# Kernel optimization log

Hardware: AMD Instinct MI355X
Metric: run time of the kernel (lower is better)

The kernel has to match this reference:

```python
import jax, jax.numpy as jnp
import numpy as np

R = 16      # num_rels
NB = 16     # num_bases
N2 = 8192   # dp2 neighbours (layer-0 sampled nodes)
N1 = 1024   # dp1 neighbours (layer-1 sampled nodes)
NOUT = 256  # output batch nodes
F = 128     # feat_size
E = 64      # embed_size
C = 32      # num_classes


def setup_inputs() -> dict:
    key = jax.random.key(0)
    ks = jax.random.split(key, 8)
    g = lambda k, sh, scale: jax.random.normal(k, sh, dtype=jnp.float32) * scale
    return {
        "X_batch": g(ks[0], (N2, F), 1.0),
        "sel_idx": jnp.arange(N2, dtype=jnp.int64) if jax.config.jax_enable_x64 else jnp.arange(N2, dtype=jnp.int32),
        "A0": g(ks[1], (N1, R * N2), 1.0 / np.sqrt(R * N2)),
        "A1": g(ks[2], (NOUT, R * N1), 1.0 / np.sqrt(R * N1)),
        "comp1": g(ks[3], (R, NB), 1.0 / np.sqrt(NB)),
        "bases1": g(ks[4], (NB, F, E), 1.0 / np.sqrt(F)),
        "comp2": g(ks[5], (R, NB), 1.0 / np.sqrt(NB)),
        "bases2": g(ks[6], (NB, E, C), 1.0 / np.sqrt(E)),
        "bias1": jnp.zeros((E,), jnp.float32),
        "bias2": jnp.zeros((C,), jnp.float32),
    }


def reference(X_batch, sel_idx, A0, A1, comp1, bases1, comp2, bases2, bias1, bias2):
    # gather the rows of X_batch corresponding to dp2 neighbours
    x = X_batch[sel_idx]                                  # [N2, F]
    # layer 1: basis-composed relation weights, relation-stacked matmul
    w1 = jnp.einsum('rb,beh->reh', comp1, bases1)         # [R, F, E]
    xw = jnp.einsum('ne,reh->rnh', x, w1)                 # [R, N2, E]
    h1 = A0 @ xw.reshape(R * N2, E)                       # [N1, E]
    h1 = jax.nn.relu(h1 + bias1)
    # layer 2
    w2 = jnp.einsum('rb,bho->rho', comp2, bases2)         # [R, E, C]
    h2 = jnp.einsum('nh,rhc->rnc', h1, w2)                # [R, N1, C]
    out = A1 @ h2.reshape(R * N1, C) + bias2              # [NOUT, C]
    return out
```

## Files before the change

kernel.cpp:

```cpp
#include <hip/hip_runtime.h>

#define RR_ 16
#define N2_ 8192
#define N1_ 1024
#define NOUT_ 256
#define F_ 128
#define E_ 64
#define C_ 32
#define KBIG_ 131072

typedef __attribute__((ext_vector_type(4))) float f32x4;
typedef __attribute__((ext_vector_type(8))) short short8;
typedef __attribute__((ext_vector_type(4))) short s16x4;

#define MFMA(a,b,c) __builtin_amdgcn_mfma_f32_16x16x32_bf16((a),(b),(c),0,0,0)

__device__ __forceinline__ unsigned short f2bf(float f) {
  unsigned int u = __builtin_bit_cast(unsigned int, f);
  u += 0x7fffu + ((u >> 16) & 1u);
  return (unsigned short)(u >> 16);
}

__device__ __forceinline__ short8 cvt8(f32x4 v0, f32x4 v1) {
  short8 r;
  r[0] = (short)f2bf(v0[0]); r[1] = (short)f2bf(v0[1]);
  r[2] = (short)f2bf(v0[2]); r[3] = (short)f2bf(v0[3]);
  r[4] = (short)f2bf(v1[0]); r[5] = (short)f2bf(v1[1]);
  r[6] = (short)f2bf(v1[2]); r[7] = (short)f2bf(v1[3]);
  return r;
}

__global__ __launch_bounds__(256) void k_prep(
    const float* __restrict__ comp1, const float* __restrict__ bases1,
    const float* __restrict__ comp2, const float* __restrict__ bases2,
    short* __restrict__ w1T, short* __restrict__ w2T)
{
  int bid = blockIdx.x, t = threadIdx.x;
  if (bid < 32) {
    int base = bid * 4096;
    for (int i = 0; i < 16; ++i) {
      int e = base + i * 256 + t;
      int r = e >> 13, rem = e & 8191;
      int h = rem >> 7, f = rem & 127;
      float s = 0.f;
      #pragma unroll
      for (int b = 0; b < 16; ++b) s += comp1[r * 16 + b] * bases1[b * 8192 + f * 64 + h];
      w1T[e] = (short)f2bf(s);
    }
  } else {
    int base = (bid - 32) * 4096;
    for (int i = 0; i < 16; ++i) {
      int e = base + i * 256 + t;
      int r = e >> 11, rem = e & 2047;
      int c = rem >> 6, h = rem & 63;
      float s = 0.f;
      #pragma unroll
      for (int b = 0; b < 16; ++b) s += comp2[r * 16 + b] * bases2[b * 2048 + h * 32 + c];
      w2T[e] = (short)f2bf(s);
    }
  }
}

__global__ __launch_bounds__(256) void k_xw(
    const float* __restrict__ X, const int* __restrict__ sel,
    const short* __restrict__ w1T, short* __restrict__ xwT)
{
  int w = blockIdx.x * 4 + (threadIdx.x >> 6);
  int lane = threadIdx.x & 63, lr = lane & 15, lg = lane >> 4;
  int r = w >> 8;
  int n0 = (w & 255) * 32;

  bool is64 = (sel[1] == 0 && sel[2] == 1);
  int i0 = is64 ? sel[2 * (n0 + lr)] : sel[n0 + lr];
  int i1 = is64 ? sel[2 * (n0 + 16 + lr)] : sel[n0 + 16 + lr];

  const short* aBase = w1T + r * 8192 + lr * 128 + 8 * lg;
  const float* b0p = X + (size_t)i0 * 128 + 8 * lg;
  const float* b1p = X + (size_t)i1 * 128 + 8 * lg;

  f32x4 acc[4][2] = {};
  #pragma unroll
  for (int ks = 0; ks < 4; ++ks) {
    short8 a[4];
    #pragma unroll
    for (int mf = 0; mf < 4; ++mf)
      a[mf] = *(const short8*)(aBase + mf * 2048 + ks * 32);
    short8 b[2];
    b[0] = cvt8(*(const f32x4*)(b0p + ks * 32), *(const f32x4*)(b0p + ks * 32 + 4));
    b[1] = cvt8(*(const f32x4*)(b1p + ks * 32), *(const f32x4*)(b1p + ks * 32 + 4));
    #pragma unroll
    for (int mf = 0; mf < 4; ++mf)
      #pragma unroll
      for (int nf = 0; nf < 2; ++nf)
        acc[mf][nf] = MFMA(a[mf], b[nf], acc[mf][nf]);
  }
  #pragma unroll
  for (int mf = 0; mf < 4; ++mf)
    #pragma unroll
    for (int nf = 0; nf < 2; ++nf)
      #pragma unroll
      for (int rr = 0; rr < 4; ++rr) {
        int h = mf * 16 + 4 * lg + rr;
        int col = r * 8192 + n0 + nf * 16 + lr;
        xwT[(size_t)h * KBIG_ + col] = (short)f2bf(acc[mf][nf][rr]);
      }
}

__global__ __launch_bounds__(256) void k_h1(
    const float* __restrict__ A0, const short* __restrict__ xwT,
    float* __restrict__ h1p)
{
  int w = blockIdx.x * 4 + (threadIdx.x >> 6);
  int lane = threadIdx.x & 63, lr = lane & 15, lg = lane >> 4;
  int mt = w >> 7;
  int ch = w & 127;
  int m0 = mt * 64;
  size_t kc = (size_t)ch * 1024;

  const float* aBase = A0 + (size_t)(m0 + lr) * KBIG_ + kc + 8 * lg;
  const short* bBase = xwT + (size_t)lr * KBIG_ + kc + 8 * lg;

  f32x4 acc[4][4] = {};
  for (int ks = 0; ks < 32; ++ks) {
    short8 a[4];
    #pragma unroll
    for (int mf = 0; mf < 4; ++mf) {
      const float* p = aBase + (size_t)mf * 16 * KBIG_ + ks * 32;
      f32x4 v0 = __builtin_nontemporal_load((const f32x4*)p);
      f32x4 v1 = __builtin_nontemporal_load((const f32x4*)p + 1);
      a[mf] = cvt8(v0, v1);
    }
    short8 b[4];
    #pragma unroll
    for (int nf = 0; nf < 4; ++nf)
      b[nf] = *(const short8*)(bBase + (size_t)nf * 16 * KBIG_ + ks * 32);
    #pragma unroll
    for (int mf = 0; mf < 4; ++mf)
      #pragma unroll
      for (int nf = 0; nf < 4; ++nf)
        acc[mf][nf] = MFMA(a[mf], b[nf], acc[mf][nf]);
  }
  float* base = h1p + (size_t)ch * 65536;
  #pragma unroll
  for (int mf = 0; mf < 4; ++mf)
    #pragma unroll
    for (int nf = 0; nf < 4; ++nf)
      #pragma unroll
      for (int rr = 0; rr < 4; ++rr)
        base[(m0 + mf * 16 + 4 * lg + rr) * 64 + nf * 16 + lr] = acc[mf][nf][rr];
}

__global__ __launch_bounds__(256) void k_red(
    const float* __restrict__ h1p, const float* __restrict__ bias1,
    short* __restrict__ h1b)
{
  int e = (blockIdx.x * 256 + threadIdx.x) * 4;
  f32x4 s = {0.f, 0.f, 0.f, 0.f};
  #pragma unroll 8
  for (int c = 0; c < 128; ++c) {
    f32x4 v = *(const f32x4*)(h1p + (size_t)c * 65536 + e);
    s += v;
  }
  int h = e & 63;
  s16x4 o;
  #pragma unroll
  for (int j = 0; j < 4; ++j) {
    float x = s[j] + bias1[h + j];
    x = x > 0.f ? x : 0.f;
    o[j] = (short)f2bf(x);
  }
  *(s16x4*)(h1b + e) = o;
}

__global__ __launch_bounds__(256) void k_h2(
    const short* __restrict__ w2T, const short* __restrict__ h1b,
    short* __restrict__ H2T)
{
  int w = blockIdx.x * 4 + (threadIdx.x >> 6);
  int lane = threadIdx.x & 63, lr = lane & 15, lg = lane >> 4;
  int r = w >> 4;
  int n0 = (w & 15) * 64;

  f32x4 acc[2][4] = {};
  #pragma unroll
  for (int ks = 0; ks < 2; ++ks) {
    short8 a[2];
    #pragma unroll
    for (int mf = 0; mf < 2; ++mf)
      a[mf] = *(const short8*)(w2T + r * 2048 + (mf * 16 + lr) * 64 + ks * 32 + 8 * lg);
    short8 b[4];
    #pragma unroll
    for (int nf = 0; nf < 4; ++nf)
      b[nf] = *(const short8*)(h1b + (size_t)(n0 + nf * 16 + lr) * 64 + ks * 32 + 8 * lg);
    #pragma unroll
    for (int mf = 0; mf < 2; ++mf)
      #pragma unroll
      for (int nf = 0; nf < 4; ++nf)
        acc[mf][nf] = MFMA(a[mf], b[nf], acc[mf][nf]);
  }
  #pragma unroll
  for (int mf = 0; mf < 2; ++mf)
    #pragma unroll
    for (int nf = 0; nf < 4; ++nf)
      #pragma unroll
      for (int rr = 0; rr < 4; ++rr) {
        int c = mf * 16 + 4 * lg + rr;
        int col = r * 1024 + n0 + nf * 16 + lr;
        H2T[(size_t)c * 16384 + col] = (short)f2bf(acc[mf][nf][rr]);
      }
}

__global__ __launch_bounds__(256) void k_out(
    const float* __restrict__ A1, const short* __restrict__ H2T,
    float* __restrict__ outp)
{
  int w = blockIdx.x * 4 + (threadIdx.x >> 6);
  int lane = threadIdx.x & 63, lr = lane & 15, lg = lane >> 4;
  int mt = w >> 7;
  int ch = w & 127;
  int m0 = mt * 64;
  size_t kc = (size_t)ch * 128;

  const float* aBase = A1 + (size_t)(m0 + lr) * 16384 + kc + 8 * lg;
  const short* bBase = H2T + (size_t)lr * 16384 + kc + 8 * lg;

  f32x4 acc[4][2] = {};
  #pragma unroll
  for (int ks = 0; ks < 4; ++ks) {
    short8 a[4];
    #pragma unroll
    for (int mf = 0; mf < 4; ++mf) {
      const float* p = aBase + (size_t)mf * 16 * 16384 + ks * 32;
      f32x4 v0 = __builtin_nontemporal_load((const f32x4*)p);
      f32x4 v1 = __builtin_nontemporal_load((const f32x4*)p + 1);
      a[mf] = cvt8(v0, v1);
    }
    short8 b[2];
    #pragma unroll
    for (int nf = 0; nf < 2; ++nf)
      b[nf] = *(const short8*)(bBase + (size_t)nf * 16 * 16384 + ks * 32);
    #pragma unroll
    for (int mf = 0; mf < 4; ++mf)
      #pragma unroll
      for (int nf = 0; nf < 2; ++nf)
        acc[mf][nf] = MFMA(a[mf], b[nf], acc[mf][nf]);
  }
  float* base = outp + (size_t)ch * 8192;
  #pragma unroll
  for (int mf = 0; mf < 4; ++mf)
    #pragma unroll
    for (int nf = 0; nf < 2; ++nf)
      #pragma unroll
      for (int rr = 0; rr < 4; ++rr)
        base[(m0 + mf * 16 + 4 * lg + rr) * 32 + nf * 16 + lr] = acc[mf][nf][rr];
}

__global__ __launch_bounds__(256) void k_outred(
    const float* __restrict__ outp, const float* __restrict__ bias2,
    float* __restrict__ out)
{
  int e = (blockIdx.x * 256 + threadIdx.x) * 4;
  f32x4 s = {0.f, 0.f, 0.f, 0.f};
  #pragma unroll 8
  for (int c = 0; c < 128; ++c) {
    f32x4 v = *(const f32x4*)(outp + (size_t)c * 8192 + e);
    s += v;
  }
  int cc = e & 31;
  f32x4 o;
  #pragma unroll
  for (int j = 0; j < 4; ++j)
    o[j] = s[j] + bias2[cc + j];
  *(f32x4*)(out + e) = o;
}

extern "C" void kernel_launch(void* const* d_in, const int* in_sizes, int n_in,
                              void* d_out, int out_size, void* d_ws, size_t ws_size,
                              hipStream_t stream) {
  (void)in_sizes; (void)n_in; (void)out_size; (void)ws_size;
  const float* X      = (const float*)d_in[0];
  const int*   sel    = (const int*)  d_in[1];
  const float* A0     = (const float*)d_in[2];
  const float* A1     = (const float*)d_in[3];
  const float* comp1  = (const float*)d_in[4];
  const float* bases1 = (const float*)d_in[5];
  const float* comp2  = (const float*)d_in[6];
  const float* bases2 = (const float*)d_in[7];
  const float* bias1  = (const float*)d_in[8];
  const float* bias2  = (const float*)d_in[9];
  float* out = (float*)d_out;

  char* ws = (char*)d_ws;
  short* w1T = (short*)(ws);
  short* w2T = (short*)(ws + 262144);
  short* xwT = (short*)(ws + 327680);
  float* h1p = (float*)(ws + 17104896);
  short* h1b = (short*)(ws + 50659328);
  short* H2T = (short*)(ws + 50790400);
  float* outp= (float*)(ws + 51838976);

  k_prep  <<<40,   256, 0, stream>>>(comp1, bases1, comp2, bases2, w1T, w2T);
  k_xw    <<<1024, 256, 0, stream>>>(X, sel, w1T, xwT);
  k_h1    <<<512,  256, 0, stream>>>(A0, xwT, h1p);
  k_red   <<<64,   256, 0, stream>>>(h1p, bias1, h1b);
  k_h2    <<<64,   256, 0, stream>>>(w2T, h1b, H2T);
  k_out   <<<128,  256, 0, stream>>>(A1, H2T, outp);
  k_outred<<<8,    256, 0, stream>>>(outp, bias2, out);
}
```

Before: 254.4 us.

## Stage A0 tiles into LDS with double-buffered async loads in k_h1

Rewrites the big A0 @ xw kernel so each block stages 64x256 fp32 tiles of A0 into double-buffered shared memory using global_load_lds, overlapping the next tile's load with MFMA work on the current one. K is split into 16 chunks instead of 128, which shrinks the partial-sum buffer and the k_red reduction, and the grid is halved. It also switches k_out's A1 loads from nontemporal to regular loads. The trade-off is fewer blocks with 128KB of LDS each (low occupancy), plus a full barrier per stage.

```diff
diff --git a/kernel.cpp b/kernel.cpp
--- a/kernel.cpp
+++ b/kernel.cpp
@@ -106,48 +106,63 @@
       }
 }
 
+__device__ __forceinline__ void stage16(const float* gbase, int s, float* ldst) {
+  #pragma unroll
+  for (int j = 0; j < 16; ++j) {
+    const float* gp = gbase + (size_t)j * KBIG_ + (size_t)s * 256;
+    __builtin_amdgcn_global_load_lds(
+        (const __attribute__((address_space(1))) void*)gp,
+        (__attribute__((address_space(3))) void*)(ldst + j * 256), 16, 0, 0);
+  }
+}
+
 __global__ __launch_bounds__(256) void k_h1(
     const float* __restrict__ A0, const short* __restrict__ xwT,
     float* __restrict__ h1p)
 {
-  int w = blockIdx.x * 4 + (threadIdx.x >> 6);
-  int lane = threadIdx.x & 63, lr = lane & 15, lg = lane >> 4;
-  int mt = w >> 7;
-  int ch = w & 127;
+  __shared__ float As[2][64][256];
+  int tid = threadIdx.x;
+  int w = tid >> 6;
+  int lane = tid & 63, lr = lane & 15, lg = lane >> 4;
+  int mt = blockIdx.x >> 4;
+  int ch = blockIdx.x & 15;
   int m0 = mt * 64;
-  size_t kc = (size_t)ch * 1024;
-
-  const float* aBase = A0 + (size_t)(m0 + lr) * KBIG_ + kc + 8 * lg;
-  const short* bBase = xwT + (size_t)lr * KBIG_ + kc + 8 * lg;
-
-  f32x4 acc[4][4] = {};
-  for (int ks = 0; ks < 32; ++ks) {
-    short8 a[4];
-    #pragma unroll
-    for (int mf = 0; mf < 4; ++mf) {
-      const float* p = aBase + (size_t)mf * 16 * KBIG_ + ks * 32;
-      f32x4 v0 = __builtin_nontemporal_load((const f32x4*)p);
-      f32x4 v1 = __builtin_nontemporal_load((const f32x4*)p + 1);
-      a[mf] = cvt8(v0, v1);
+  size_t kc = (size_t)ch * 8192;
+
+  const float* gbase = A0 + (size_t)(m0 + 16 * w) * KBIG_ + kc + (size_t)lane * 4;
+  const short* bb    = xwT + (size_t)lr * KBIG_ + kc + 8 * lg;
+
+  f32x4 acc[4] = {};
+
+  stage16(gbase, 0, &As[0][16 * w][0]);
+  __syncthreads();
+
+  for (int s = 0; s < 32; ++s) {
+    int cur = s & 1;
+    if (s + 1 < 32)
+      stage16(gbase, s + 1, &As[cur ^ 1][16 * w][0]);
+
+    const float* lrow = &As[cur][16 * w + lr][0] + 8 * lg;
+    #pragma unroll
+    for (int ks = 0; ks < 8; ++ks) {
+      f32x4 v0 = *(const f32x4*)(lrow + ks * 32);
+      f32x4 v1 = *(const f32x4*)(lrow + ks * 32 + 4);
+      short8 a = cvt8(v0, v1);
+      #pragma unroll
+      for (int nf = 0; nf < 4; ++nf) {
+        short8 b = *(const short8*)(bb + (size_t)nf * 16 * KBIG_ + s * 256 + ks * 32);
+        acc[nf] = MFMA(a, b, acc[nf]);
+      }
     }
-    short8 b[4];
-    #pragma unroll
-    for (int nf = 0; nf < 4; ++nf)
-      b[nf] = *(const short8*)(bBase + (size_t)nf * 16 * KBIG_ + ks * 32);
-    #pragma unroll
-    for (int mf = 0; mf < 4; ++mf)
-      #pragma unroll
-      for (int nf = 0; nf < 4; ++nf)
-        acc[mf][nf] = MFMA(a[mf], b[nf], acc[mf][nf]);
-  }
-  float* base = h1p + (size_t)ch * 65536;
-  #pragma unroll
-  for (int mf = 0; mf < 4; ++mf)
-    #pragma unroll
-    for (int nf = 0; nf < 4; ++nf)
-      #pragma unroll
-      for (int rr = 0; rr < 4; ++rr)
-        base[(m0 + mf * 16 + 4 * lg + rr) * 64 + nf * 16 + lr] = acc[mf][nf][rr];
+    __syncthreads();
+  }
+
+  float* base = h1p + (size_t)ch * 65536 + (size_t)(m0 + 16 * w) * 64;
+  #pragma unroll
+  for (int nf = 0; nf < 4; ++nf)
+    #pragma unroll
+    for (int rr = 0; rr < 4; ++rr)
+      base[(4 * lg + rr) * 64 + nf * 16 + lr] = acc[nf][rr];
 }
 
 __global__ __launch_bounds__(256) void k_red(
@@ -156,8 +171,8 @@
 {
   int e = (blockIdx.x * 256 + threadIdx.x) * 4;
   f32x4 s = {0.f, 0.f, 0.f, 0.f};
-  #pragma unroll 8
-  for (int c = 0; c < 128; ++c) {
+  #pragma unroll
+  for (int c = 0; c < 16; ++c) {
     f32x4 v = *(const f32x4*)(h1p + (size_t)c * 65536 + e);
     s += v;
   }
@@ -231,8 +246,8 @@
     #pragma unroll
     for (int mf = 0; mf < 4; ++mf) {
       const float* p = aBase + (size_t)mf * 16 * 16384 + ks * 32;
-      f32x4 v0 = __builtin_nontemporal_load((const f32x4*)p);
-      f32x4 v1 = __builtin_nontemporal_load((const f32x4*)p + 1);
+      f32x4 v0 = *(const f32x4*)p;
+      f32x4 v1 = *((const f32x4*)p + 1);
       a[mf] = cvt8(v0, v1);
     }
     short8 b[2];
@@ -301,7 +316,7 @@
 
   k_prep  <<<40,   256, 0, stream>>>(comp1, bases1, comp2, bases2, w1T, w2T);
   k_xw    <<<1024, 256, 0, stream>>>(X, sel, w1T, xwT);
-  k_h1    <<<512,  256, 0, stream>>>(A0, xwT, h1p);
+  k_h1    <<<256,  256, 0, stream>>>(A0, xwT, h1p);
   k_red   <<<64,   256, 0, stream>>>(h1p, bias1, h1b);
   k_h2    <<<64,   256, 0, stream>>>(w2T, h1b, H2T);
   k_out   <<<128,  256, 0, stream>>>(A1, H2T, outp);
```

New measurement: 426.5 us. 67.7% more time.
